# Kernel tuning notes

Hardware: AMD Instinct MI355X
Metric: run time of the kernel (lower is better)

## Reference

```python
import jax, jax.numpy as jnp
import numpy as np

WINDOW_SIZE = 128

def setup_inputs() -> dict:
    key = jax.random.key(0)
    kq, kk, kv = jax.random.split(key, 3)
    B, S, D = 4, 4096, 128
    q = jax.random.normal(kq, (B, S, D), dtype=jnp.float32)
    k = jax.random.normal(kk, (B, S, D), dtype=jnp.float32)
    v = jax.random.normal(kv, (B, S, D), dtype=jnp.float32)
    return {"q": q, "k": k, "v": v}

def reference(q, k, v):
    B, S, D = q.shape
    q = q / jnp.sqrt(jnp.asarray(D, q.dtype))
    # band mask: tril(window_size-1) & triu(-(window_size-1)) == |i - j| <= window_size-1
    i = jax.lax.broadcasted_iota(jnp.int32, (S, S), 0)
    j = jax.lax.broadcasted_iota(jnp.int32, (S, S), 1)
    mask = jnp.abs(i - j) <= (WINDOW_SIZE - 1)
    scores = jnp.einsum('bqd,bkd->bqk', q, k)  # [B,S,S]
    scores = jnp.where(mask, scores, jnp.asarray(-1e9, scores.dtype))
    weights = jax.nn.softmax(scores, axis=-1)
    return jnp.einsum('bqk,bkd->bqd', weights, v)
```

## Files before the change

kernel.cpp:

```cpp
#include <hip/hip_runtime.h>


typedef __attribute__((ext_vector_type(8))) _Float16 half8;
typedef __attribute__((ext_vector_type(2))) __fp16 fp16x2;
typedef __attribute__((ext_vector_type(4))) float floatx4;

#define MFMA_F16(a, b, c) __builtin_amdgcn_mfma_f32_16x16x32_f16(a, b, c, 0, 0, 0)

constexpr int S_ = 4096, D_ = 128, W_ = 127;
constexpr int BQ = 64, BK = 64;
constexpr int KST = 136;
constexpr int PST = 72;
constexpr int OST = 132;

union SMem {
  struct {
    _Float16 Kh[2][BK * KST];
    _Float16 Vt[2][D_ * 64];
    _Float16 Ps[4][16 * PST];
  } a;
  struct {
    float Om[8][16 * OST];
    float l_[8][16];
  } b;
};

__device__ __forceinline__ unsigned pk2(float a, float b) {
  union { fp16x2 h; unsigned u; } cvt;
  cvt.h = __builtin_amdgcn_cvt_pkrtz(a, b);
  return cvt.u;
}

__global__ __launch_bounds__(512, 2)
void swa_v5_kernel(const float* __restrict__ qg, const float* __restrict__ kg,
                   const float* __restrict__ vg, float* __restrict__ og)
{
  __shared__ __align__(16) SMem sm;
  const int tid  = threadIdx.x;
  const int lane = tid & 63;
  const int wave = tid >> 6;
  const int lx   = lane & 15;
  const int quad = lane >> 4;
  const int tile = wave & 3;
  const int par  = wave >> 2;

  const int bid = blockIdx.x;
  const int lid = (bid & 7) * 32 + (bid >> 3);
  const int bb  = lid >> 6;
  const int q0  = (lid & 63) * BQ;

  const float* qb = qg + (size_t)bb * S_ * D_;
  const float* kb = kg + (size_t)bb * S_ * D_;
  const float* vb = vg + (size_t)bb * S_ * D_;
  float*       ob = og + (size_t)bb * S_ * D_;

  const int qrow = q0 + 16 * tile + lx;
  half8 qh[4], ql[4];
#pragma unroll
  for (int ks = 0; ks < 4; ++ks) {
    const float* p = qb + (size_t)qrow * D_ + 32 * ks + 8 * quad;
#pragma unroll
    for (int j = 0; j < 8; ++j) {
      float f = p[j];
      _Float16 h = (_Float16)f;
      qh[ks][j] = h;
      ql[ks][j] = (_Float16)(f - (float)h);
    }
  }

  floatx4 o[8];
#pragma unroll
  for (int dt = 0; dt < 8; ++dt) o[dt] = (floatx4){0.f, 0.f, 0.f, 0.f};
  float lp[4] = {0.f, 0.f, 0.f, 0.f};

  const int kstart = (q0 > W_) ? (q0 - W_) : 0;
  int kend = q0 + BQ - 1 + W_;
  if (kend > S_ - 1) kend = S_ - 1;
  const int c0 = kstart >> 6, c1 = kend >> 6;

  const int ilo = q0 + 16 * tile, ihi = ilo + 15;
  const float C1 = 0.12751727f, C2 = -5.7707802f;

  const int sh   = tid >> 8;
  const int kr16 = tid >> 4, c8 = tid & 15;
  const int t2   = tid & 255;
  const int vr   = t2 & 7, vc = t2 >> 3;

  float4 pf[8];
  if (sh == 0) {
#pragma unroll
    for (int j = 0; j < 4; ++j) {
      const float* src = kb + (size_t)(c0 * BK + kr16 + 16 * j) * D_ + 8 * c8;
      pf[2 * j]     = *(const float4*)(src);
      pf[2 * j + 1] = *(const float4*)(src + 4);
    }
  } else {
#pragma unroll
    for (int u = 0; u < 8; ++u)
      pf[u] = *(const float4*)(vb + (size_t)(c0 * BK + 8 * vr + u) * D_ + 4 * vc);
  }

  for (int c = c0; c <= c1; ++c) {
    const int buf = c & 1;
    if (sh == 0) {
#pragma unroll
      for (int j = 0; j < 4; ++j) {
        const float* f0 = (const float*)&pf[2 * j];
        const float* f1 = (const float*)&pf[2 * j + 1];
        uint4 kh8;
        kh8.x = pk2(f0[0], f0[1]);
        kh8.y = pk2(f0[2], f0[3]);
        kh8.z = pk2(f1[0], f1[1]);
        kh8.w = pk2(f1[2], f1[3]);
        *(uint4*)(&sm.a.Kh[buf][(kr16 + 16 * j) * KST + 8 * c8]) = kh8;
      }
    } else {
#pragma unroll
      for (int i = 0; i < 4; ++i) {
        uint4 tv;
        tv.x = pk2(((const float*)&pf[0])[i], ((const float*)&pf[1])[i]);
        tv.y = pk2(((const float*)&pf[2])[i], ((const float*)&pf[3])[i]);
        tv.z = pk2(((const float*)&pf[4])[i], ((const float*)&pf[5])[i]);
        tv.w = pk2(((const float*)&pf[6])[i], ((const float*)&pf[7])[i]);
        const int d = 4 * vc + i;
        const int g = vr ^ (d & 7);
        *(uint4*)(&sm.a.Vt[buf][d * 64 + 8 * g]) = tv;
      }
    }
    if (c < c1) {
      if (sh == 0) {
#pragma unroll
        for (int j = 0; j < 4; ++j) {
          const float* src = kb + (size_t)((c + 1) * BK + kr16 + 16 * j) * D_ + 8 * c8;
          pf[2 * j]     = *(const float4*)(src);
          pf[2 * j + 1] = *(const float4*)(src + 4);
        }
      } else {
#pragma unroll
        for (int u = 0; u < 8; ++u)
          pf[u] = *(const float4*)(vb + (size_t)((c + 1) * BK + 8 * vr + u) * D_ + 4 * vc);
      }
    }
    __syncthreads();

    if (((c - c0) & 1) != par) continue;
    const int kc = c * BK;
    if (kc + BK - 1 < ilo - W_ || kc > ihi + W_) continue;

    floatx4 acc[4];
#pragma unroll
    for (int ct = 0; ct < 4; ++ct) acc[ct] = (floatx4){0.f, 0.f, 0.f, 0.f};
#pragma unroll
    for (int ks = 0; ks < 4; ++ks) {
      const int dof = 32 * ks + 8 * quad;
      half8 b0 = *(const half8*)(&sm.a.Kh[buf][(lx)      * KST + dof]);
      half8 b1 = *(const half8*)(&sm.a.Kh[buf][(16 + lx) * KST + dof]);
      half8 b2 = *(const half8*)(&sm.a.Kh[buf][(32 + lx) * KST + dof]);
      half8 b3 = *(const half8*)(&sm.a.Kh[buf][(48 + lx) * KST + dof]);
      acc[0] = MFMA_F16(qh[ks], b0, acc[0]);
      acc[1] = MFMA_F16(qh[ks], b1, acc[1]);
      acc[2] = MFMA_F16(qh[ks], b2, acc[2]);
      acc[3] = MFMA_F16(qh[ks], b3, acc[3]);
      acc[0] = MFMA_F16(ql[ks], b0, acc[0]);
      acc[1] = MFMA_F16(ql[ks], b1, acc[1]);
      acc[2] = MFMA_F16(ql[ks], b2, acc[2]);
      acc[3] = MFMA_F16(ql[ks], b3, acc[3]);
    }

    const int ibase = q0 + 16 * tile + 4 * quad;
#pragma unroll
    for (int r = 0; r < 4; ++r) {
      const int i = ibase + r;
      float psum = 0.f;
#pragma unroll
      for (int ct = 0; ct < 4; ++ct) {
        const int col = kc + 16 * ct + lx;
        const bool v = (unsigned)(col - i + W_) <= (unsigned)(2 * W_);
        const float e = __builtin_amdgcn_exp2f(__builtin_fmaf(acc[ct][r], C1, C2));
        const float p = v ? e : 0.f;
        psum += p;
        sm.a.Ps[tile][(4 * quad + r) * PST + 16 * ct + lx] = (_Float16)p;
      }
      lp[r] += psum;
    }
    asm volatile("s_waitcnt lgkmcnt(0)" ::: "memory");
    half8 pa0 = *(const half8*)(&sm.a.Ps[tile][lx * PST + 8 * quad]);
    half8 pa1 = *(const half8*)(&sm.a.Ps[tile][lx * PST + 32 + 8 * quad]);

#pragma unroll
    for (int dt = 0; dt < 8; ++dt) {
      const int d = 16 * dt + lx;
      const int gs = lx & 7;
      half8 v0 = *(const half8*)(&sm.a.Vt[buf][d * 64 + 8 * (quad ^ gs)]);
      half8 v1 = *(const half8*)(&sm.a.Vt[buf][d * 64 + 8 * ((4 + quad) ^ gs)]);
      o[dt] = MFMA_F16(pa0, v0, o[dt]);
      o[dt] = MFMA_F16(pa1, v1, o[dt]);
    }
  }

#pragma unroll
  for (int r = 0; r < 4; ++r) {
    float s = lp[r];
    s += __shfl_xor(s, 1);
    s += __shfl_xor(s, 2);
    s += __shfl_xor(s, 4);
    s += __shfl_xor(s, 8);
    lp[r] = s;
  }

  __syncthreads();
#pragma unroll
  for (int dt = 0; dt < 8; ++dt)
#pragma unroll
    for (int r = 0; r < 4; ++r)
      sm.b.Om[wave][(4 * quad + r) * OST + 16 * dt + lx] = o[dt][r];
  if (lx == 0) {
#pragma unroll
    for (int r = 0; r < 4; ++r) sm.b.l_[wave][4 * quad + r] = lp[r];
  }
  __syncthreads();

  const int row = tid >> 3, cd = tid & 7;
  const int tl = row >> 4, r16 = row & 15;
  const float inv = 1.f / (sm.b.l_[tl][r16] + sm.b.l_[tl + 4][r16]);
  const float* Oa = &sm.b.Om[tl][r16 * OST + 16 * cd];
  const float* Ob = &sm.b.Om[tl + 4][r16 * OST + 16 * cd];
  float* dst = ob + (size_t)(q0 + row) * D_ + 16 * cd;
#pragma unroll
  for (int t = 0; t < 4; ++t) {
    float4 xa = *(const float4*)(Oa + 4 * t);
    float4 xb = *(const float4*)(Ob + 4 * t);
    float4 r4;
    r4.x = (xa.x + xb.x) * inv;
    r4.y = (xa.y + xb.y) * inv;
    r4.z = (xa.z + xb.z) * inv;
    r4.w = (xa.w + xb.w) * inv;
    *(float4*)(dst + 4 * t) = r4;
  }
}

extern "C" void kernel_launch(void* const* d_in, const int* in_sizes, int n_in,
                              void* d_out, int out_size, void* d_ws, size_t ws_size,
                              hipStream_t stream) {
  const float* q = (const float*)d_in[0];
  const float* k = (const float*)d_in[1];
  const float* v = (const float*)d_in[2];
  float* out = (float*)d_out;

  const int B = in_sizes[0] / (S_ * D_);
  dim3 grid(B * (S_ / BQ));
  dim3 block(512);
  swa_v5_kernel<<<grid, block, 0, stream>>>(q, k, v, out);
}
```

Before: 90.42 us.

## Pre-convert K/V to swizzled fp16 in workspace and async-load tiles into LDS

Adds a prep kernel that converts K to fp16 with an XOR-swizzled layout and V to transposed, swizzled fp16 tiles, written to the workspace. The attention kernel then streams these pre-laid-out tiles straight into LDS with global_load_lds double buffering. This removes per-block fp32 loads, conversion and register staging, and halves the K/V bytes each block reads. In exchange it adds a second launch plus an extra full pass over K and V, and the workspace must be large enough to hold both fp16 copies.

Result: faster. 88.59 us (-2.0%).

```diff
diff --git a/kernel.cpp b/kernel.cpp
--- a/kernel.cpp
+++ b/kernel.cpp
@@ -9,14 +9,13 @@
 
 constexpr int S_ = 4096, D_ = 128, W_ = 127;
 constexpr int BQ = 64, BK = 64;
-constexpr int KST = 136;
 constexpr int PST = 72;
 constexpr int OST = 132;
 
 union SMem {
   struct {
-    _Float16 Kh[2][BK * KST];
-    _Float16 Vt[2][D_ * 64];
+    _Float16 Kh[2][BK * D_];
+    _Float16 Vt[2][D_ * BK];
     _Float16 Ps[4][16 * PST];
   } a;
   struct {
@@ -26,14 +25,69 @@
 };
 
 __device__ __forceinline__ unsigned pk2(float a, float b) {
-  union { fp16x2 h; unsigned u; } cvt;
-  cvt.h = __builtin_amdgcn_cvt_pkrtz(a, b);
-  return cvt.u;
+  union { fp16x2 h; unsigned u; } c;
+  c.h = __builtin_amdgcn_cvt_pkrtz(a, b);
+  return c.u;
+}
+
+__device__ __forceinline__ void gll16(const _Float16* g, _Float16* l) {
+  __builtin_amdgcn_global_load_lds(
+      (const __attribute__((address_space(1))) void*)g,
+      (__attribute__((address_space(3))) void*)l, 16, 0, 0);
+}
+
+__global__ __launch_bounds__(256, 4)
+void prep_kernel(const float* __restrict__ kg, const float* __restrict__ vg,
+                 _Float16* __restrict__ K16, _Float16* __restrict__ Vt16)
+{
+  __shared__ __align__(16) _Float16 Vs[BK * D_];
+  const int t  = threadIdx.x;
+  const int bb = blockIdx.x >> 6;
+  const int c  = blockIdx.x & 63;
+  const size_t base = ((size_t)bb * S_ + c * 64) * D_;
+
+#pragma unroll
+  for (int j = 0; j < 4; ++j) {
+    const int id = t + 256 * j;
+    const int s = id >> 4, blk = id & 15;
+    const float* src = kg + base + s * D_ + blk * 8;
+    float4 a  = *(const float4*)src;
+    float4 b2 = *(const float4*)(src + 4);
+    uint4 w;
+    w.x = pk2(a.x, a.y);  w.y = pk2(a.z, a.w);
+    w.z = pk2(b2.x, b2.y); w.w = pk2(b2.z, b2.w);
+    *(uint4*)(K16 + base + s * D_ + 8 * (blk ^ (s & 7))) = w;
+  }
+
+  const int vr = t >> 5, vc = t & 31;
+  float4 vf[8];
+#pragma unroll
+  for (int u = 0; u < 8; ++u)
+    vf[u] = *(const float4*)(vg + base + (8 * vr + u) * D_ + 4 * vc);
+#pragma unroll
+  for (int i = 0; i < 4; ++i) {
+    uint4 tv;
+    tv.x = pk2(((const float*)&vf[0])[i], ((const float*)&vf[1])[i]);
+    tv.y = pk2(((const float*)&vf[2])[i], ((const float*)&vf[3])[i]);
+    tv.z = pk2(((const float*)&vf[4])[i], ((const float*)&vf[5])[i]);
+    tv.w = pk2(((const float*)&vf[6])[i], ((const float*)&vf[7])[i]);
+    const int d = 4 * vc + i;
+    *(uint4*)(&Vs[d * 64 + 8 * (vr ^ (d & 7))]) = tv;
+  }
+  __syncthreads();
+  _Float16* vdst = Vt16 + (size_t)(bb * 64 + c) * (D_ * 64);
+#pragma unroll
+  for (int i = 0; i < 4; ++i) {
+    const int id2 = t + 256 * i;
+    *(uint4*)(vdst + id2 * 8) = *(const uint4*)(&Vs[id2 * 8]);
+  }
 }
 
 __global__ __launch_bounds__(512, 2)
-void swa_v5_kernel(const float* __restrict__ qg, const float* __restrict__ kg,
-                   const float* __restrict__ vg, float* __restrict__ og)
+void swa_v6_kernel(const float* __restrict__ qg,
+                   const _Float16* __restrict__ K16,
+                   const _Float16* __restrict__ Vt16,
+                   float* __restrict__ og)
 {
   __shared__ __align__(16) SMem sm;
   const int tid  = threadIdx.x;
@@ -50,8 +104,6 @@
   const int q0  = (lid & 63) * BQ;
 
   const float* qb = qg + (size_t)bb * S_ * D_;
-  const float* kb = kg + (size_t)bb * S_ * D_;
-  const float* vb = vg + (size_t)bb * S_ * D_;
   float*       ob = og + (size_t)bb * S_ * D_;
 
   const int qrow = q0 + 16 * tile + lx;
@@ -81,67 +133,36 @@
   const int ilo = q0 + 16 * tile, ihi = ilo + 15;
   const float C1 = 0.12751727f, C2 = -5.7707802f;
 
-  const int sh   = tid >> 8;
-  const int kr16 = tid >> 4, c8 = tid & 15;
-  const int t2   = tid & 255;
-  const int vr   = t2 & 7, vc = t2 >> 3;
-
-  float4 pf[8];
-  if (sh == 0) {
-#pragma unroll
-    for (int j = 0; j < 4; ++j) {
-      const float* src = kb + (size_t)(c0 * BK + kr16 + 16 * j) * D_ + 8 * c8;
-      pf[2 * j]     = *(const float4*)(src);
-      pf[2 * j + 1] = *(const float4*)(src + 4);
-    }
-  } else {
-#pragma unroll
-    for (int u = 0; u < 8; ++u)
-      pf[u] = *(const float4*)(vb + (size_t)(c0 * BK + 8 * vr + u) * D_ + 4 * vc);
+  const int wk = (wave < 4) ? wave : (wave - 4);
+
+  {
+    const int b0 = c0 & 1;
+    const _Float16* kcb = K16 + ((size_t)bb * S_ + c0 * 64) * D_;
+    const _Float16* vcb = Vt16 + (size_t)(bb * 64 + c0) * (D_ * 64);
+#pragma unroll
+    for (int i = 0; i < 4; ++i) {
+      const int ofs = (wk * 4 + i) * 512;
+      if (wave < 4) gll16(kcb + ofs + lane * 8, &sm.a.Kh[b0][ofs]);
+      else          gll16(vcb + ofs + lane * 8, &sm.a.Vt[b0][ofs]);
+    }
   }
 
   for (int c = c0; c <= c1; ++c) {
     const int buf = c & 1;
-    if (sh == 0) {
-#pragma unroll
-      for (int j = 0; j < 4; ++j) {
-        const float* f0 = (const float*)&pf[2 * j];
-        const float* f1 = (const float*)&pf[2 * j + 1];
-        uint4 kh8;
-        kh8.x = pk2(f0[0], f0[1]);
-        kh8.y = pk2(f0[2], f0[3]);
-        kh8.z = pk2(f1[0], f1[1]);
-        kh8.w = pk2(f1[2], f1[3]);
-        *(uint4*)(&sm.a.Kh[buf][(kr16 + 16 * j) * KST + 8 * c8]) = kh8;
+    asm volatile("s_waitcnt vmcnt(0)" ::: "memory");
+    __builtin_amdgcn_s_barrier();
+    asm volatile("" ::: "memory");
+
+    if (c < c1) {
+      const _Float16* kcb = K16 + ((size_t)bb * S_ + (c + 1) * 64) * D_;
+      const _Float16* vcb = Vt16 + (size_t)(bb * 64 + (c + 1)) * (D_ * 64);
+#pragma unroll
+      for (int i = 0; i < 4; ++i) {
+        const int ofs = (wk * 4 + i) * 512;
+        if (wave < 4) gll16(kcb + ofs + lane * 8, &sm.a.Kh[buf ^ 1][ofs]);
+        else          gll16(vcb + ofs + lane * 8, &sm.a.Vt[buf ^ 1][ofs]);
       }
-    } else {
-#pragma unroll
-      for (int i = 0; i < 4; ++i) {
-        uint4 tv;
-        tv.x = pk2(((const float*)&pf[0])[i], ((const float*)&pf[1])[i]);
-        tv.y = pk2(((const float*)&pf[2])[i], ((const float*)&pf[3])[i]);
-        tv.z = pk2(((const float*)&pf[4])[i], ((const float*)&pf[5])[i]);
-        tv.w = pk2(((const float*)&pf[6])[i], ((const float*)&pf[7])[i]);
-        const int d = 4 * vc + i;
-        const int g = vr ^ (d & 7);
-        *(uint4*)(&sm.a.Vt[buf][d * 64 + 8 * g]) = tv;
-      }
-    }
-    if (c < c1) {
-      if (sh == 0) {
-#pragma unroll
-        for (int j = 0; j < 4; ++j) {
-          const float* src = kb + (size_t)((c + 1) * BK + kr16 + 16 * j) * D_ + 8 * c8;
-          pf[2 * j]     = *(const float4*)(src);
-          pf[2 * j + 1] = *(const float4*)(src + 4);
-        }
-      } else {
-#pragma unroll
-        for (int u = 0; u < 8; ++u)
-          pf[u] = *(const float4*)(vb + (size_t)((c + 1) * BK + 8 * vr + u) * D_ + 4 * vc);
-      }
-    }
-    __syncthreads();
+    }
 
     if (((c - c0) & 1) != par) continue;
     const int kc = c * BK;
@@ -152,19 +173,14 @@
     for (int ct = 0; ct < 4; ++ct) acc[ct] = (floatx4){0.f, 0.f, 0.f, 0.f};
 #pragma unroll
     for (int ks = 0; ks < 4; ++ks) {
-      const int dof = 32 * ks + 8 * quad;
-      half8 b0 = *(const half8*)(&sm.a.Kh[buf][(lx)      * KST + dof]);
-      half8 b1 = *(const half8*)(&sm.a.Kh[buf][(16 + lx) * KST + dof]);
-      half8 b2 = *(const half8*)(&sm.a.Kh[buf][(32 + lx) * KST + dof]);
-      half8 b3 = *(const half8*)(&sm.a.Kh[buf][(48 + lx) * KST + dof]);
-      acc[0] = MFMA_F16(qh[ks], b0, acc[0]);
-      acc[1] = MFMA_F16(qh[ks], b1, acc[1]);
-      acc[2] = MFMA_F16(qh[ks], b2, acc[2]);
-      acc[3] = MFMA_F16(qh[ks], b3, acc[3]);
-      acc[0] = MFMA_F16(ql[ks], b0, acc[0]);
-      acc[1] = MFMA_F16(ql[ks], b1, acc[1]);
-      acc[2] = MFMA_F16(ql[ks], b2, acc[2]);
-      acc[3] = MFMA_F16(ql[ks], b3, acc[3]);
+#pragma unroll
+      for (int ct = 0; ct < 4; ++ct) {
+        const int row = 16 * ct + lx;
+        half8 bfr = *(const half8*)(
+            &sm.a.Kh[buf][row * D_ + 8 * ((4 * ks + quad) ^ (lx & 7))]);
+        acc[ct] = MFMA_F16(qh[ks], bfr, acc[ct]);
+        acc[ct] = MFMA_F16(ql[ks], bfr, acc[ct]);
+      }
     }
 
     const int ibase = q0 + 16 * tile + 4 * quad;
@@ -190,9 +206,8 @@
 #pragma unroll
     for (int dt = 0; dt < 8; ++dt) {
       const int d = 16 * dt + lx;
-      const int gs = lx & 7;
-      half8 v0 = *(const half8*)(&sm.a.Vt[buf][d * 64 + 8 * (quad ^ gs)]);
-      half8 v1 = *(const half8*)(&sm.a.Vt[buf][d * 64 + 8 * ((4 + quad) ^ gs)]);
+      half8 v0 = *(const half8*)(&sm.a.Vt[buf][d * 64 + 8 * (quad ^ (d & 7))]);
+      half8 v1 = *(const half8*)(&sm.a.Vt[buf][d * 64 + 8 * ((4 + quad) ^ (d & 7))]);
       o[dt] = MFMA_F16(pa0, v0, o[dt]);
       o[dt] = MFMA_F16(pa1, v1, o[dt]);
     }
@@ -248,7 +263,9 @@
   float* out = (float*)d_out;
 
   const int B = in_sizes[0] / (S_ * D_);
-  dim3 grid(B * (S_ / BQ));
-  dim3 block(512);
-  swa_v5_kernel<<<grid, block, 0, stream>>>(q, k, v, out);
-}
+  _Float16* K16  = (_Float16*)d_ws;
+  _Float16* Vt16 = (_Float16*)d_ws + (size_t)B * S_ * D_;
+
+  prep_kernel<<<dim3(B * (S_ / BK)), dim3(256), 0, stream>>>(k, v, K16, Vt16);
+  swa_v6_kernel<<<dim3(B * (S_ / BQ)), dim3(512), 0, stream>>>(q, K16, Vt16, out);
+}
```
